# Kernel optimization log

Measured on AMD Instinct MI355X. Metric: run time of the kernel, lower is better.

## Reference

```python
import jax, jax.numpy as jnp
import numpy as np

H = 8        # num attention heads
DH = 160     # head dim (hidden_size // H)
HS = 1280    # hidden_size
CAD = 768    # cross_attention_dim
R = 4        # LoRA rank
LORA_SCALE = 1.0  # `scale` forward arg (default 1.0)


def setup_inputs() -> dict:
    key = jax.random.key(0)
    ks = jax.random.split(key, 16)
    rn = lambda k, s, std=0.02: (jax.random.normal(k, s) * std).astype(jnp.float32)
    return {
        "hidden_states": jax.random.normal(ks[0], (8, 4096, HS), jnp.float32),
        "encoder_hidden_states": jax.random.normal(ks[1], (8, 77, CAD), jnp.float32),
        # base attention projections (nn.Linear weight layout: [out, in])
        "Wq": rn(ks[2], (HS, HS)),
        "Wk": rn(ks[3], (HS, CAD)),
        "Wv": rn(ks[4], (HS, CAD)),
        "Wo": rn(ks[5], (HS, HS)),
        "bo": jnp.zeros((HS,), jnp.float32),
        # LoRA down/up pairs (down std ~ 1/rank; up nonzero so grads flow)
        "q_down": rn(ks[6], (R, HS), 0.25), "q_up": rn(ks[7], (HS, R)),
        "k_down": rn(ks[8], (R, CAD), 0.25), "k_up": rn(ks[9], (HS, R)),
        "v_down": rn(ks[10], (R, CAD), 0.25), "v_up": rn(ks[11], (HS, R)),
        "o_down": rn(ks[12], (R, HS), 0.25), "o_up": rn(ks[13], (HS, R)),
    }


def reference(hidden_states, encoder_hidden_states, Wq, Wk, Wv, Wo, bo,
              q_down, q_up, k_down, k_up, v_down, v_up, o_down, o_up):
    B, S, _ = hidden_states.shape
    T = encoder_hidden_states.shape[1]
    lora = lambda x, d, u: (x @ d.T) @ u.T  # LoRALinearLayer: up(down(x))

    q = hidden_states @ Wq.T + LORA_SCALE * lora(hidden_states, q_down, q_up)
    k = encoder_hidden_states @ Wk.T + LORA_SCALE * lora(encoder_hidden_states, k_down, k_up)
    v = encoder_hidden_states @ Wv.T + LORA_SCALE * lora(encoder_hidden_states, v_down, v_up)

    q = q.reshape(B, S, H, DH)
    k = k.reshape(B, T, H, DH)
    v = v.reshape(B, T, H, DH)

    # attn.get_attention_scores: scaled QK^T, softmax (no mask)
    inv_sqrt_d = jnp.asarray(1.0 / np.sqrt(DH), q.dtype)
    scores = jnp.einsum('bshd,bthd->bhst', q, k) * inv_sqrt_d
    probs = jax.nn.softmax(scores, axis=-1)
    o = jnp.einsum('bhst,bthd->bshd', probs, v).reshape(B, S, H * DH)

    # to_out[0] (Linear with bias) + LoRA on the same input; to_out[1] dropout = identity (eval)
    return o @ Wo.T + bo + LORA_SCALE * lora(o, o_down, o_up)
```

## Files before the change

kernel.cpp:

```cpp
#include <hip/hip_runtime.h>
#include <hip/hip_bf16.h>
#include <stdint.h>

typedef short bf16x8 __attribute__((ext_vector_type(8)));
typedef float f32x4 __attribute__((ext_vector_type(4)));

#define DEVI static __device__ __forceinline__

DEVI ushort f2bf(float f) {
  union { float f; uint32_t u; } v; v.f = f;
  uint32_t u = v.u;
  return (ushort)((u + 0x7fffu + ((u >> 16) & 1u)) >> 16);
}

DEVI void gload16(const void* g, void* l) {
  __builtin_amdgcn_global_load_lds((const __attribute__((address_space(1))) void*)g,
                                   (__attribute__((address_space(3))) void*)l,
                                   16, 0, 0);
}

#define SB() __builtin_amdgcn_sched_barrier(0)
#define BAR() __builtin_amdgcn_s_barrier()
#define MFMA(a, b, c) __builtin_amdgcn_mfma_f32_16x16x32_bf16((a), (b), (c), 0, 0, 0)

DEVI int pair_src_row(int c, int* k8) {
  int pair = c >> 3;
  int s = (c & 7) ^ (pair & 7);
  *k8 = s >> 1;
  return pair * 2 + (s & 1);
}
DEVI int pair_frag_off(int r, int k8) {
  int p = (k8 * 2 + (r & 1)) ^ ((r >> 1) & 7);
  return (r >> 1) * 64 + p * 8;
}

__global__ __launch_bounds__(256) void fold_t(
    const float* __restrict__ W, const float* __restrict__ up,
    const float* __restrict__ down, ushort* __restrict__ outT, float scale)
{
  __shared__ ushort tile[64][66];
  const int o0 = blockIdx.x * 64, i0 = blockIdx.y * 64;
  const int lo = threadIdx.x >> 6;
  const int li = threadIdx.x & 63;
#pragma unroll
  for (int r = 0; r < 16; ++r) {
    int o = o0 + r * 4 + lo;
    int i = i0 + li;
    float v = W[(long)o * 1280 + i];
#pragma unroll
    for (int q = 0; q < 4; ++q) v += up[o * 4 + q] * down[q * 1280 + i];
    tile[li][r * 4 + lo] = f2bf(v * scale);
  }
  __syncthreads();
#pragma unroll
  for (int r = 0; r < 16; ++r) {
    int i = i0 + r * 4 + lo;
    outT[(long)i * 1280 + o0 + li] = tile[r * 4 + lo][li];
  }
}

__global__ __launch_bounds__(256) void smalls(
    const float* __restrict__ ehs, ushort* __restrict__ ehs_bf,
    const float* __restrict__ Wk, const float* __restrict__ k_up, const float* __restrict__ k_down,
    const float* __restrict__ Wv, const float* __restrict__ v_up, const float* __restrict__ v_down,
    ushort* __restrict__ Wkv,
    const float* __restrict__ Wo, const float* __restrict__ o_up, const float* __restrict__ o_down,
    ushort* __restrict__ Wo_bf, ushort* __restrict__ Nt)
{
  const int b = blockIdx.x;
  const int tid = threadIdx.x;
  if (b < 231) {
    int idx = b * 256 + tid;
    if (idx < 59136) {
      const float4* p = (const float4*)(ehs + (long)idx * 8);
      float4 a = p[0], c = p[1];
      union { ushort us[8]; uint4 v; } r;
      r.us[0] = f2bf(a.x); r.us[1] = f2bf(a.y); r.us[2] = f2bf(a.z); r.us[3] = f2bf(a.w);
      r.us[4] = f2bf(c.x); r.us[5] = f2bf(c.y); r.us[6] = f2bf(c.z); r.us[7] = f2bf(c.w);
      *(uint4*)(ehs_bf + (long)idx * 8) = r.v;
    }
  } else if (b < 4071) {
    int idx = (b - 231) * 256 + tid;
    int o = idx / 768, i = idx - o * 768;
    float v = Wk[idx];
#pragma unroll
    for (int q = 0; q < 4; ++q) v += k_up[o * 4 + q] * k_down[q * 768 + i];
    Wkv[idx] = f2bf(v);
  } else if (b < 7911) {
    int idx = (b - 4071) * 256 + tid;
    int o = idx / 768, i = idx - o * 768;
    float v = Wv[idx];
#pragma unroll
    for (int q = 0; q < 4; ++q) v += v_up[o * 4 + q] * v_down[q * 768 + i];
    Wkv[983040 + idx] = f2bf(v);
  } else if (b < 14311) {
    int idx = (b - 7911) * 256 + tid;
    int o = idx / 1280, i = idx - o * 1280;
    float v = Wo[idx];
#pragma unroll
    for (int q = 0; q < 4; ++q) v += o_up[o * 4 + q] * o_down[q * 1280 + i];
    Wo_bf[idx] = f2bf(v);
  } else {
    int idx = (b - 14311) * 256 + tid;
    int bb = idx / (1280 * 24);
    int rem = idx % (1280 * 24);
    int j = rem / 24, q = rem % 24;
    int h = q / 3, t = 77 + q % 3;
    Nt[(long)bb * 1280 * 640 + (long)j * 640 + h * 80 + t] = 0;
  }
}


DEVI void gemm_bt_body(int bx, int by, int z,
    const ushort* __restrict__ A, long sA0, long sA1, int lda, int validM,
    const ushort* __restrict__ B, long sB0, long sB1, int ldb, int validN,
    float* __restrict__ C32, ushort* __restrict__ C16, long sC0, long sC1, int ldc,
    const float* __restrict__ bias, int K, ushort* As, ushort* Bs)
{
  const ushort* Ab = A + (long)(z >> 3) * sA0 + (long)(z & 7) * sA1;
  const ushort* Bb = B + (long)(z >> 3) * sB0 + (long)(z & 7) * sB1;
  const int m0 = bx * 128;
  const int n0 = by * 128;
  const int tid = threadIdx.x;
  const int lane = tid & 63;
  const int wid = tid >> 6;

  const int c0 = tid;
  const int arow0 = min(m0 + (c0 >> 2), validM - 1);
  const int arow1 = min(m0 + (c0 >> 2) + 64, validM - 1);
  const int brow0 = min(n0 + (c0 >> 2), validN - 1);
  const int brow1 = min(n0 + (c0 >> 2) + 64, validN - 1);
  const int seg = (c0 & 3) * 8;

  const int wr = (wid >> 1) * 64;
  const int wc = (wid & 1) * 64;
  const int frow = lane & 15;
  const int fk = (lane >> 4) * 8;

  f32x4 acc[4][4] = {};

  for (int kt = 0; kt < K; kt += 32) {
    gload16(Ab + (long)arow0 * lda + kt + seg, As + c0 * 8);
    gload16(Ab + (long)arow1 * lda + kt + seg, As + (c0 + 256) * 8);
    gload16(Bb + (long)brow0 * ldb + kt + seg, Bs + c0 * 8);
    gload16(Bb + (long)brow1 * ldb + kt + seg, Bs + (c0 + 256) * 8);
    __syncthreads();

    bf16x8 af[4], bfr[4];
#pragma unroll
    for (int m = 0; m < 4; ++m)
      af[m] = *(const bf16x8*)(As + (wr + m * 16 + frow) * 32 + fk);
#pragma unroll
    for (int n = 0; n < 4; ++n)
      bfr[n] = *(const bf16x8*)(Bs + (wc + n * 16 + frow) * 32 + fk);
#pragma unroll
    for (int m = 0; m < 4; ++m)
#pragma unroll
      for (int n = 0; n < 4; ++n)
        acc[m][n] = MFMA(af[m], bfr[n], acc[m][n]);
    __syncthreads();
  }

  const long cb = (long)(z >> 3) * sC0 + (long)(z & 7) * sC1;
  const int crow = m0 + wr + (lane >> 4) * 4;
  const int ccol = n0 + wc + (lane & 15);
#pragma unroll
  for (int m = 0; m < 4; ++m)
#pragma unroll
    for (int n = 0; n < 4; ++n)
#pragma unroll
      for (int j = 0; j < 4; ++j) {
        int r = crow + m * 16 + j;
        int c = ccol + n * 16;
        if (r < validM && c < validN) {
          float v = acc[m][n][j];
          if (bias) v += bias[c];
          if (C32) C32[cb + (long)r * ldc + c] = v;
          else     C16[cb + (long)r * ldc + c] = f2bf(v);
        }
      }
}

__global__ __launch_bounds__(256) void gemm_bt(
    const ushort* A, long sA0, long sA1, int lda, int validM,
    const ushort* B, long sB0, long sB1, int ldb, int validN,
    float* C32, ushort* C16, long sC0, long sC1, int ldc,
    const float* bias, int K)
{
  __shared__ ushort As[128 * 32];
  __shared__ ushort Bs[128 * 32];
  gemm_bt_body(blockIdx.x, blockIdx.y, blockIdx.z,
               A, sA0, sA1, lda, validM, B, sB0, sB1, ldb, validN,
               C32, C16, sC0, sC1, ldc, bias, K, As, Bs);
}

__global__ __launch_bounds__(256) void gemm_mtnt(
    const ushort* __restrict__ kv_bf, const ushort* __restrict__ WqT,
    const ushort* __restrict__ Wo_bf, ushort* __restrict__ Mt, ushort* __restrict__ Nt)
{
  __shared__ ushort As[128 * 32];
  __shared__ ushort Bs[128 * 32];
  const int x = blockIdx.x, z = blockIdx.z;
  if (x < 10) {
    gemm_bt_body(x, 0, z, Wo_bf, 0, 160, 1280, 1280,
                 kv_bf + 1280, 77L * 2560, 160, 2560, 77,
                 nullptr, Nt, 1280L * 640, 80, 640, nullptr, 160, As, Bs);
  } else {
    gemm_bt_body(0, x - 10, z, kv_bf, 77L * 2560, 160, 2560, 77,
                 WqT, 0, 160, 1280, 1280,
                 nullptr, Mt, 640L * 1280, 77L * 1280, 1280, nullptr, 160, As, Bs);
  }
}

__global__ __launch_bounds__(256, 3) void score_softmax(
    const float* __restrict__ hsf, const ushort* __restrict__ Mt,
    ushort* __restrict__ probs)
{
  __shared__ ushort lds[22528];

  const int z = blockIdx.z;
  const int s0 = blockIdx.x * 128;
  const int h0 = blockIdx.y * 2;
  const int tid = threadIdx.x;
  const int lane = tid & 63;
  const int wid = tid >> 6;
  const int wM = wid >> 1;
  const int wN = wid & 1;
  const int l15 = lane & 15;
  const int l4 = lane >> 4;

  const int ar = tid >> 1, ah = tid & 1;
  const float* Ag = hsf + ((long)z * 4096 + s0 + ar) * 1280 + 16 * ah;
  const int awoff0 = pair_frag_off(ar, 2 * ah);
  const int awoff1 = pair_frag_off(ar, 2 * ah + 1);

  const ushort* Bg = Mt + (long)z * (640L * 1280);
  long bsrc[3]; int bdst[3];
#pragma unroll
  for (int j = 0; j < 3; ++j) {
    int c = j * 256 + tid, k8;
    int rb = pair_src_row(c, &k8);
    int hh = h0 + (rb >= 96);
    int tt = min(rb - 96 * (rb >= 96), 76);
    bsrc[j] = (long)(hh * 77 + tt) * 1280 + k8 * 8;
    bdst[j] = 4096 + c * 8;
  }

  int aoff[4], boff[6];
#pragma unroll
  for (int m = 0; m < 4; ++m)
    aoff[m] = pair_frag_off(wM * 64 + m * 16 + l15, l4);
#pragma unroll
  for (int n = 0; n < 6; ++n)
    boff[n] = 4096 + pair_frag_off(wN * 96 + n * 16 + l15, l4);

  f32x4 acc[4][6] = {};
  float4 pa0, pa1, pa2, pa3;

#define SS_LOADA(kt) { const float* p_ = Ag + (kt); \
    pa0 = *(const float4*)(p_);     pa1 = *(const float4*)(p_ + 4); \
    pa2 = *(const float4*)(p_ + 8); pa3 = *(const float4*)(p_ + 12); }
#define SS_GLB(bb, kt) { _Pragma("unroll") for (int j = 0; j < 3; ++j) \
    gload16(Bg + bsrc[j] + (kt), &lds[(bb) + bdst[j]]); }
#define SS_CVTW(bb) { \
    union { ushort us[8]; bf16x8 v; } c0_, c1_; \
    c0_.us[0]=f2bf(pa0.x); c0_.us[1]=f2bf(pa0.y); c0_.us[2]=f2bf(pa0.z); c0_.us[3]=f2bf(pa0.w); \
    c0_.us[4]=f2bf(pa1.x); c0_.us[5]=f2bf(pa1.y); c0_.us[6]=f2bf(pa1.z); c0_.us[7]=f2bf(pa1.w); \
    c1_.us[0]=f2bf(pa2.x); c1_.us[1]=f2bf(pa2.y); c1_.us[2]=f2bf(pa2.z); c1_.us[3]=f2bf(pa2.w); \
    c1_.us[4]=f2bf(pa3.x); c1_.us[5]=f2bf(pa3.y); c1_.us[6]=f2bf(pa3.z); c1_.us[7]=f2bf(pa3.w); \
    *(bf16x8*)(&lds[(bb) + awoff0]) = c0_.v; \
    *(bf16x8*)(&lds[(bb) + awoff1]) = c1_.v; }

  SS_LOADA(0)
  SB();
  SS_GLB(0, 0)
  SB();
  SS_CVTW(0)
  asm volatile("s_waitcnt lgkmcnt(0)" ::: "memory");

  for (int t = 0; t < 40; ++t) {
    const int base = (t & 1) * 10240;
    const int nb = 10240 - base;
    if (t + 1 < 40) {
      const int kt1 = (t + 1) * 32;
      SS_LOADA(kt1)
      SB();
      SS_GLB(nb, kt1)
      asm volatile("s_waitcnt vmcnt(7)" ::: "memory");
    } else {
      asm volatile("s_waitcnt vmcnt(0)" ::: "memory");
    }
    SB(); BAR(); SB();
    bf16x8 av[4], bv[6];
#pragma unroll
    for (int m = 0; m < 4; ++m) av[m] = *(const bf16x8*)(&lds[base + aoff[m]]);
#pragma unroll
    for (int n = 0; n < 6; ++n) bv[n] = *(const bf16x8*)(&lds[base + boff[n]]);
    __builtin_amdgcn_s_setprio(1);
#pragma unroll
    for (int m = 0; m < 4; ++m)
#pragma unroll
      for (int n = 0; n < 6; ++n)
        acc[m][n] = MFMA(av[m], bv[n], acc[m][n]);
    __builtin_amdgcn_s_setprio(0);
    SB();
    if (t + 1 < 40) { SS_CVTW(nb) }
    asm volatile("s_waitcnt lgkmcnt(0)" ::: "memory");
    SB(); BAR();
  }
#undef SS_LOADA
#undef SS_GLB
#undef SS_CVTW

#pragma unroll
  for (int m = 0; m < 4; ++m)
#pragma unroll
    for (int j = 0; j < 4; ++j) {
      float mx = -1e30f;
#pragma unroll
      for (int n = 0; n < 6; ++n)
        if (n * 16 + l15 < 77) mx = fmaxf(mx, acc[m][n][j]);
#pragma unroll
      for (int o = 8; o; o >>= 1) mx = fmaxf(mx, __shfl_xor(mx, o));
      float sum = 0.f;
#pragma unroll
      for (int n = 0; n < 6; ++n) {
        float e = (n * 16 + l15 < 77) ? __expf(acc[m][n][j] - mx) : 0.f;
        acc[m][n][j] = e;
        sum += e;
      }
#pragma unroll
      for (int o = 8; o; o >>= 1) sum += __shfl_xor(sum, o);
      float inv = 1.f / sum;
#pragma unroll
      for (int n = 0; n < 6; ++n) acc[m][n][j] *= inv;
    }

  __syncthreads();
  ushort* pw = lds + wid * 5632;
#pragma unroll
  for (int m = 0; m < 4; ++m)
#pragma unroll
    for (int n = 0; n < 5; ++n)
#pragma unroll
      for (int j = 0; j < 4; ++j)
        pw[(m * 16 + l4 * 4 + j) * 88 + n * 16 + l15] = f2bf(acc[m][n][j]);

  const uint* pw32 = (const uint*)pw;
  uint* probs32 = (uint*)probs;
  const int head = h0 + wN;
  const long sbase = (long)z * 4096 + s0 + wM * 64;
#pragma unroll 4
  for (int k = 0; k < 40; ++k) {
    int f2 = k * 64 + lane;
    int r = f2 / 40;
    int tp = f2 - r * 40;
    probs32[(sbase + r) * 320 + head * 40 + tp] = pw32[r * 44 + tp];
  }
}

__global__ __launch_bounds__(256, 4) void gemm_out(
    const ushort* __restrict__ P, const ushort* __restrict__ Nt,
    float* __restrict__ C, const float* __restrict__ bias)
{
  __shared__ ushort lds[17408];

  const int z = blockIdx.z;
  const ushort* Ab = P + (long)z * (4096L * 640) + (long)blockIdx.x * 128 * 640;
  const ushort* Bb = Nt + (long)z * (1280L * 640) + (long)blockIdx.y * 128 * 640;
  const int tid = threadIdx.x;
  const int lane = tid & 63;
  const int wid = tid >> 6;
  const int wM = wid >> 1;
  const int wN = wid & 1;
  const int l15 = lane & 15;
  const int l4 = lane >> 4;

  long asrc[2]; int adst[2], bdst[2];
#pragma unroll
  for (int j = 0; j < 2; ++j) {
    int c = j * 256 + tid, k8;
    int r = pair_src_row(c, &k8);
    asrc[j] = (long)r * 640 + k8 * 8;
    adst[j] = c * 8;
    bdst[j] = 4096 + c * 8;
  }

  int aoff[4], boff[4];
#pragma unroll
  for (int m = 0; m < 4; ++m)
    aoff[m] = pair_frag_off(wM * 64 + m * 16 + l15, l4);
#pragma unroll
  for (int n = 0; n < 4; ++n)
    boff[n] = 4096 + pair_frag_off(wN * 64 + n * 16 + l15, l4);

  f32x4 acc[4][4] = {};

#define OG_STAGE(bb, kt) { \
    _Pragma("unroll") for (int j = 0; j < 2; ++j) gload16(Ab + asrc[j] + (kt), &lds[(bb) + adst[j]]); \
    _Pragma("unroll") for (int j = 0; j < 2; ++j) gload16(Bb + asrc[j] + (kt), &lds[(bb) + bdst[j]]); }

  OG_STAGE(0, 0)

  for (int t = 0; t < 20; ++t) {
    const int base = (t & 1) * 8192;
    if (t + 1 < 20) {
      OG_STAGE(8192 - base, (t + 1) * 32)
      asm volatile("s_waitcnt vmcnt(4)" ::: "memory");
    } else {
      asm volatile("s_waitcnt vmcnt(0)" ::: "memory");
    }
    SB(); BAR(); SB();
    bf16x8 av[4], bv[4];
#pragma unroll
    for (int m = 0; m < 4; ++m) av[m] = *(const bf16x8*)(&lds[base + aoff[m]]);
#pragma unroll
    for (int n = 0; n < 4; ++n) bv[n] = *(const bf16x8*)(&lds[base + boff[n]]);
    __builtin_amdgcn_s_setprio(1);
#pragma unroll
    for (int m = 0; m < 4; ++m)
#pragma unroll
      for (int n = 0; n < 4; ++n)
        acc[m][n] = MFMA(av[m], bv[n], acc[m][n]);
    __builtin_amdgcn_s_setprio(0);
    SB(); BAR();
  }
#undef OG_STAGE

  __syncthreads();
  float* pw = (float*)lds + wid * 1088;
  const int ccol = blockIdx.y * 128 + wN * 64;
  const float4 bv4 = *(const float4*)(bias + ccol + l15 * 4);
  const long crow0 = (long)z * 4096 + blockIdx.x * 128 + wM * 64;
#pragma unroll
  for (int m = 0; m < 4; ++m) {
#pragma unroll
    for (int n = 0; n < 4; ++n)
#pragma unroll
      for (int j = 0; j < 4; ++j)
        pw[(l4 * 4 + j) * 68 + n * 16 + l15] = acc[m][n][j];
    asm volatile("s_waitcnt lgkmcnt(0)" ::: "memory"); SB();
#pragma unroll
    for (int pass = 0; pass < 4; ++pass) {
      int r = pass * 4 + l4;
      float4 v = *(const float4*)(pw + r * 68 + l15 * 4);
      v.x += bv4.x; v.y += bv4.y; v.z += bv4.z; v.w += bv4.w;
      *(float4*)(C + (crow0 + m * 16 + r) * 1280 + ccol + l15 * 4) = v;
    }
    asm volatile("s_waitcnt lgkmcnt(0)" ::: "memory"); SB();
  }
}

extern "C" void kernel_launch(void* const* d_in, const int* in_sizes, int n_in,
                              void* d_out, int out_size, void* d_ws, size_t ws_size,
                              hipStream_t stream) {
  (void)in_sizes; (void)n_in; (void)out_size; (void)ws_size;
  const float* hs     = (const float*)d_in[0];
  const float* ehs    = (const float*)d_in[1];
  const float* Wq     = (const float*)d_in[2];
  const float* Wk     = (const float*)d_in[3];
  const float* Wv     = (const float*)d_in[4];
  const float* Wo     = (const float*)d_in[5];
  const float* bo     = (const float*)d_in[6];
  const float* q_down = (const float*)d_in[7];
  const float* q_up   = (const float*)d_in[8];
  const float* k_down = (const float*)d_in[9];
  const float* k_up   = (const float*)d_in[10];
  const float* v_down = (const float*)d_in[11];
  const float* v_up   = (const float*)d_in[12];
  const float* o_down = (const float*)d_in[13];
  const float* o_up   = (const float*)d_in[14];

  char* w = (char*)d_ws;
  size_t off = 0;
  auto alloc = [&](size_t b) { char* p = w + off; off = (off + b + 255) & ~(size_t)255; return p; };
  ushort* ehs_bf = (ushort*)alloc(616L * 768 * 2);
  ushort* WqT    = (ushort*)alloc(1280L * 1280 * 2);
  ushort* Wkv    = (ushort*)alloc(2560L * 768 * 2);
  ushort* Wo_bf  = (ushort*)alloc(1280L * 1280 * 2);
  ushort* kv_bf  = (ushort*)alloc(616L * 2560 * 2);
  ushort* Mt     = (ushort*)alloc(8L * 640 * 1280 * 2);
  ushort* Nt     = (ushort*)alloc(8L * 1280 * 640 * 2);
  ushort* probs  = (ushort*)alloc(8L * 4096 * 640 * 2);
  float*  outp   = (float*)d_out;
  const float invs = 0.07905694150420949f;

  fold_t<<<dim3(20, 20), 256, 0, stream>>>(Wq, q_up, q_down, WqT, invs);
  smalls<<<15271, 256, 0, stream>>>(ehs, ehs_bf,
      Wk, k_up, k_down, Wv, v_up, v_down, Wkv,
      Wo, o_up, o_down, Wo_bf, Nt);
  gemm_bt<<<dim3(5, 20, 1), 256, 0, stream>>>(ehs_bf, 0, 0, 768, 616,
      Wkv, 0, 0, 768, 2560, nullptr, kv_bf, 0, 0, 2560, nullptr, 768);
  gemm_mtnt<<<dim3(20, 1, 64), 256, 0, stream>>>(kv_bf, WqT, Wo_bf, Mt, Nt);
  score_softmax<<<dim3(32, 4, 8), 256, 0, stream>>>(hs, Mt, probs);
  gemm_out<<<dim3(32, 10, 8), 256, 0, stream>>>(probs, Nt, outp, bo);
}
```

Baseline: 285.2 us.

## Prefetch fp32 A tiles two steps ahead and use packed bf16 conversion

In score_softmax, the fp32 hidden-state A tile is now loaded two k-steps ahead into alternating register sets, while B still prefetches one step ahead. This gives global loads more time to land before conversion. Conversion uses the v_cvt_pk_bf16_f32 instruction in place of the manual rounding, and each thread now loads a pair-swizzled source row so its LDS store is a contiguous 16-byte write. The cost is extra live registers for the second prefetch buffer, which could hurt occupancy under launch_bounds(256,3).

```diff
diff --git a/kernel.cpp b/kernel.cpp
--- a/kernel.cpp
+++ b/kernel.cpp
@@ -11,6 +11,12 @@
   union { float f; uint32_t u; } v; v.f = f;
   uint32_t u = v.u;
   return (ushort)((u + 0x7fffu + ((u >> 16) & 1u)) >> 16);
+}
+
+DEVI uint cvtpk(float lo, float hi) {
+  uint r;
+  asm("v_cvt_pk_bf16_f32 %0, %1, %2" : "=v"(r) : "v"(lo), "v"(hi));
+  return r;
 }
 
 DEVI void gload16(const void* g, void* l) {
@@ -229,10 +235,12 @@
   const int l15 = lane & 15;
   const int l4 = lane >> 4;
 
-  const int ar = tid >> 1, ah = tid & 1;
-  const float* Ag = hsf + ((long)z * 4096 + s0 + ar) * 1280 + 16 * ah;
-  const int awoff0 = pair_frag_off(ar, 2 * ah);
-  const int awoff1 = pair_frag_off(ar, 2 * ah + 1);
+  const float* Ag = hsf + ((long)z * 4096 + s0) * 1280;
+  int ak0, ak1;
+  const int ar0 = pair_src_row(tid, &ak0);
+  const int ar1 = pair_src_row(tid + 256, &ak1);
+  const long asrc0 = (long)ar0 * 1280 + ak0 * 8;
+  const long asrc1 = (long)ar1 * 1280 + ak1 * 8;
 
   const ushort* Bg = Mt + (long)z * (640L * 1280);
   long bsrc[3]; int bdst[3];
@@ -255,59 +263,64 @@
     boff[n] = 4096 + pair_frag_off(wN * 96 + n * 16 + l15, l4);
 
   f32x4 acc[4][6] = {};
-  float4 pa0, pa1, pa2, pa3;
-
-#define SS_LOADA(kt) { const float* p_ = Ag + (kt); \
-    pa0 = *(const float4*)(p_);     pa1 = *(const float4*)(p_ + 4); \
-    pa2 = *(const float4*)(p_ + 8); pa3 = *(const float4*)(p_ + 12); }
+  float4 pa0 = {}, pa1 = {}, pa2 = {}, pa3 = {};
+  float4 pb0 = {}, pb1 = {}, pb2 = {}, pb3 = {};
+
+#define SS_LOADA(S0, S1, S2, S3, kt) { \
+    S0 = *(const float4*)(Ag + asrc0 + (kt)); S1 = *(const float4*)(Ag + asrc0 + (kt) + 4); \
+    S2 = *(const float4*)(Ag + asrc1 + (kt)); S3 = *(const float4*)(Ag + asrc1 + (kt) + 4); }
 #define SS_GLB(bb, kt) { _Pragma("unroll") for (int j = 0; j < 3; ++j) \
     gload16(Bg + bsrc[j] + (kt), &lds[(bb) + bdst[j]]); }
-#define SS_CVTW(bb) { \
-    union { ushort us[8]; bf16x8 v; } c0_, c1_; \
-    c0_.us[0]=f2bf(pa0.x); c0_.us[1]=f2bf(pa0.y); c0_.us[2]=f2bf(pa0.z); c0_.us[3]=f2bf(pa0.w); \
-    c0_.us[4]=f2bf(pa1.x); c0_.us[5]=f2bf(pa1.y); c0_.us[6]=f2bf(pa1.z); c0_.us[7]=f2bf(pa1.w); \
-    c1_.us[0]=f2bf(pa2.x); c1_.us[1]=f2bf(pa2.y); c1_.us[2]=f2bf(pa2.z); c1_.us[3]=f2bf(pa2.w); \
-    c1_.us[4]=f2bf(pa3.x); c1_.us[5]=f2bf(pa3.y); c1_.us[6]=f2bf(pa3.z); c1_.us[7]=f2bf(pa3.w); \
-    *(bf16x8*)(&lds[(bb) + awoff0]) = c0_.v; \
-    *(bf16x8*)(&lds[(bb) + awoff1]) = c1_.v; }
-
-  SS_LOADA(0)
+#define SS_CVTW(S0, S1, S2, S3, bb) { uint4 u_; \
+    u_.x = cvtpk(S0.x, S0.y); u_.y = cvtpk(S0.z, S0.w); \
+    u_.z = cvtpk(S1.x, S1.y); u_.w = cvtpk(S1.z, S1.w); \
+    *(uint4*)(&lds[(bb) + tid * 8]) = u_; \
+    u_.x = cvtpk(S2.x, S2.y); u_.y = cvtpk(S2.z, S2.w); \
+    u_.z = cvtpk(S3.x, S3.y); u_.w = cvtpk(S3.z, S3.w); \
+    *(uint4*)(&lds[(bb) + 2048 + tid * 8]) = u_; }
+
+#define SS_STEP(t, I0, I1, I2, I3, C0, C1, C2, C3) { \
+    const int base_ = ((t) & 1) * 10240; \
+    const int nb_ = 10240 - base_; \
+    if ((t) + 2 < 40) { \
+      SS_LOADA(I0, I1, I2, I3, ((t) + 2) * 32) \
+      SB(); \
+      SS_GLB(nb_, ((t) + 1) * 32) \
+      asm volatile("s_waitcnt vmcnt(7)" ::: "memory"); \
+    } else if ((t) + 1 < 40) { \
+      SS_GLB(nb_, ((t) + 1) * 32) \
+      asm volatile("s_waitcnt vmcnt(3)" ::: "memory"); \
+    } else { \
+      asm volatile("s_waitcnt vmcnt(0)" ::: "memory"); \
+    } \
+    SB(); BAR(); SB(); \
+    bf16x8 av_[4], bv_[6]; \
+    _Pragma("unroll") for (int m = 0; m < 4; ++m) av_[m] = *(const bf16x8*)(&lds[base_ + aoff[m]]); \
+    _Pragma("unroll") for (int n = 0; n < 6; ++n) bv_[n] = *(const bf16x8*)(&lds[base_ + boff[n]]); \
+    __builtin_amdgcn_s_setprio(1); \
+    _Pragma("unroll") for (int m = 0; m < 4; ++m) \
+      _Pragma("unroll") for (int n = 0; n < 6; ++n) \
+        acc[m][n] = MFMA(av_[m], bv_[n], acc[m][n]); \
+    __builtin_amdgcn_s_setprio(0); \
+    SB(); \
+    if ((t) + 1 < 40) { SS_CVTW(C0, C1, C2, C3, nb_) } \
+    asm volatile("s_waitcnt lgkmcnt(0)" ::: "memory"); \
+    SB(); BAR(); }
+
+  SS_LOADA(pa0, pa1, pa2, pa3, 0)
   SB();
   SS_GLB(0, 0)
   SB();
-  SS_CVTW(0)
+  SS_CVTW(pa0, pa1, pa2, pa3, 0)
+  SS_LOADA(pa0, pa1, pa2, pa3, 32)
+  SB();
   asm volatile("s_waitcnt lgkmcnt(0)" ::: "memory");
 
-  for (int t = 0; t < 40; ++t) {
-    const int base = (t & 1) * 10240;
-    const int nb = 10240 - base;
-    if (t + 1 < 40) {
-      const int kt1 = (t + 1) * 32;
-      SS_LOADA(kt1)
-      SB();
-      SS_GLB(nb, kt1)
-      asm volatile("s_waitcnt vmcnt(7)" ::: "memory");
-    } else {
-      asm volatile("s_waitcnt vmcnt(0)" ::: "memory");
-    }
-    SB(); BAR(); SB();
-    bf16x8 av[4], bv[6];
-#pragma unroll
-    for (int m = 0; m < 4; ++m) av[m] = *(const bf16x8*)(&lds[base + aoff[m]]);
-#pragma unroll
-    for (int n = 0; n < 6; ++n) bv[n] = *(const bf16x8*)(&lds[base + boff[n]]);
-    __builtin_amdgcn_s_setprio(1);
-#pragma unroll
-    for (int m = 0; m < 4; ++m)
-#pragma unroll
-      for (int n = 0; n < 6; ++n)
-        acc[m][n] = MFMA(av[m], bv[n], acc[m][n]);
-    __builtin_amdgcn_s_setprio(0);
-    SB();
-    if (t + 1 < 40) { SS_CVTW(nb) }
-    asm volatile("s_waitcnt lgkmcnt(0)" ::: "memory");
-    SB(); BAR();
-  }
+  for (int tt = 0; tt < 20; ++tt) {
+    SS_STEP(2 * tt,     pb0, pb1, pb2, pb3, pa0, pa1, pa2, pa3)
+    SS_STEP(2 * tt + 1, pa0, pa1, pa2, pa3, pb0, pb1, pb2, pb3)
+  }
+#undef SS_STEP
 #undef SS_LOADA
 #undef SS_GLB
 #undef SS_CVTW
```

After: 325.3 us. 14.1% more time.

## Pre-convert hidden states to bf16 and pad Mt to 80 rows per head

Applied to the files above, without the earlier changes.

A separate pass now converts hidden_states from fp32 to bf16, so score_softmax can stage both operands straight into LDS with direct global-to-LDS loads instead of loading fp32 into registers and converting inline. Mt is repacked with 80 rows per head, padding rows zeroed in the smalls kernel. The B tile therefore shrinks from 96 to 80 columns, which cuts MFMA work and LDS per block. The cost is an extra kernel that reads and writes the whole activation tensor.

```diff
diff --git a/kernel.cpp b/kernel.cpp
--- a/kernel.cpp
+++ b/kernel.cpp
@@ -32,6 +32,19 @@
 DEVI int pair_frag_off(int r, int k8) {
   int p = (k8 * 2 + (r & 1)) ^ ((r >> 1) & 7);
   return (r >> 1) * 64 + p * 8;
+}
+
+__global__ __launch_bounds__(256) void cvt_hs(const float* __restrict__ in,
+                                              ushort* __restrict__ out) {
+  const long step = 2048L * 256;
+  for (long idx = (long)blockIdx.x * 256 + threadIdx.x; idx < 5242880; idx += step) {
+    const float4* p = (const float4*)(in + idx * 8);
+    float4 a = p[0], b = p[1];
+    union { ushort us[8]; uint4 v; } r;
+    r.us[0] = f2bf(a.x); r.us[1] = f2bf(a.y); r.us[2] = f2bf(a.z); r.us[3] = f2bf(a.w);
+    r.us[4] = f2bf(b.x); r.us[5] = f2bf(b.y); r.us[6] = f2bf(b.z); r.us[7] = f2bf(b.w);
+    *(uint4*)(out + idx * 8) = r.v;
+  }
 }
 
 __global__ __launch_bounds__(256) void fold_t(
@@ -65,7 +78,7 @@
     const float* __restrict__ Wv, const float* __restrict__ v_up, const float* __restrict__ v_down,
     ushort* __restrict__ Wkv,
     const float* __restrict__ Wo, const float* __restrict__ o_up, const float* __restrict__ o_down,
-    ushort* __restrict__ Wo_bf, ushort* __restrict__ Nt)
+    ushort* __restrict__ Wo_bf, ushort* __restrict__ Nt, ushort* __restrict__ Mt)
 {
   const int b = blockIdx.x;
   const int tid = threadIdx.x;
@@ -100,13 +113,21 @@
 #pragma unroll
     for (int q = 0; q < 4; ++q) v += o_up[o * 4 + q] * o_down[q * 1280 + i];
     Wo_bf[idx] = f2bf(v);
-  } else {
+  } else if (b < 15271) {
     int idx = (b - 14311) * 256 + tid;
     int bb = idx / (1280 * 24);
     int rem = idx % (1280 * 24);
     int j = rem / 24, q = rem % 24;
     int h = q / 3, t = 77 + q % 3;
     Nt[(long)bb * 1280 * 640 + (long)j * 640 + h * 80 + t] = 0;
+  } else {
+    int idx = (b - 15271) * 256 + tid;
+    int bb = idx / 30720;
+    int rem = idx % 30720;
+    int h = rem / 3840;
+    int q = rem % 3840;
+    int p = q / 1280, i = q % 1280;
+    Mt[(long)bb * 819200 + (long)(h * 80 + 77 + p) * 1280 + i] = 0;
   }
 }
 
@@ -208,15 +229,15 @@
   } else {
     gemm_bt_body(0, x - 10, z, kv_bf, 77L * 2560, 160, 2560, 77,
                  WqT, 0, 160, 1280, 1280,
-                 nullptr, Mt, 640L * 1280, 77L * 1280, 1280, nullptr, 160, As, Bs);
+                 nullptr, Mt, 819200, 102400, 1280, nullptr, 160, As, Bs);
   }
 }
 
 __global__ __launch_bounds__(256, 3) void score_softmax(
-    const float* __restrict__ hsf, const ushort* __restrict__ Mt,
+    const ushort* __restrict__ hsb, const ushort* __restrict__ Mt,
     ushort* __restrict__ probs)
 {
-  __shared__ ushort lds[22528];
+  __shared__ ushort lds[23040];
 
   const int z = blockIdx.z;
   const int s0 = blockIdx.x * 128;
@@ -228,89 +249,67 @@
   const int wN = wid & 1;
   const int l15 = lane & 15;
   const int l4 = lane >> 4;
-
-  const int ar = tid >> 1, ah = tid & 1;
-  const float* Ag = hsf + ((long)z * 4096 + s0 + ar) * 1280 + 16 * ah;
-  const int awoff0 = pair_frag_off(ar, 2 * ah);
-  const int awoff1 = pair_frag_off(ar, 2 * ah + 1);
-
-  const ushort* Bg = Mt + (long)z * (640L * 1280);
-  long bsrc[3]; int bdst[3];
-#pragma unroll
-  for (int j = 0; j < 3; ++j) {
-    int c = j * 256 + tid, k8;
-    int rb = pair_src_row(c, &k8);
-    int hh = h0 + (rb >= 96);
-    int tt = min(rb - 96 * (rb >= 96), 76);
-    bsrc[j] = (long)(hh * 77 + tt) * 1280 + k8 * 8;
-    bdst[j] = 4096 + c * 8;
-  }
-
-  int aoff[4], boff[6];
+  const bool xb = tid < 128;
+
+  const ushort* Ag = hsb + ((long)z * 4096 + s0) * 1280;
+  int ak0, ak1;
+  const int ar0 = pair_src_row(tid, &ak0);
+  const int ar1 = pair_src_row(tid + 256, &ak1);
+  const long asrc0 = (long)ar0 * 1280 + ak0 * 8;
+  const long asrc1 = (long)ar1 * 1280 + ak1 * 8;
+  const ushort* Bg = Mt + (long)z * 819200 + (long)h0 * 80 * 1280;
+  int bk0, bk1, bk2;
+  const int br0 = pair_src_row(tid, &bk0);
+  const int br1 = pair_src_row(tid + 256, &bk1);
+  const int br2 = pair_src_row(tid + 512, &bk2);
+  const long bsrc0 = (long)br0 * 1280 + bk0 * 8;
+  const long bsrc1 = (long)br1 * 1280 + bk1 * 8;
+  const long bsrc2 = (long)br2 * 1280 + bk2 * 8;
+
+  int aoff[4], boff[5];
 #pragma unroll
   for (int m = 0; m < 4; ++m)
     aoff[m] = pair_frag_off(wM * 64 + m * 16 + l15, l4);
 #pragma unroll
-  for (int n = 0; n < 6; ++n)
-    boff[n] = 4096 + pair_frag_off(wN * 96 + n * 16 + l15, l4);
-
-  f32x4 acc[4][6] = {};
-  float4 pa0, pa1, pa2, pa3;
-
-#define SS_LOADA(kt) { const float* p_ = Ag + (kt); \
-    pa0 = *(const float4*)(p_);     pa1 = *(const float4*)(p_ + 4); \
-    pa2 = *(const float4*)(p_ + 8); pa3 = *(const float4*)(p_ + 12); }
-#define SS_GLB(bb, kt) { _Pragma("unroll") for (int j = 0; j < 3; ++j) \
-    gload16(Bg + bsrc[j] + (kt), &lds[(bb) + bdst[j]]); }
-#define SS_CVTW(bb) { \
-    union { ushort us[8]; bf16x8 v; } c0_, c1_; \
-    c0_.us[0]=f2bf(pa0.x); c0_.us[1]=f2bf(pa0.y); c0_.us[2]=f2bf(pa0.z); c0_.us[3]=f2bf(pa0.w); \
-    c0_.us[4]=f2bf(pa1.x); c0_.us[5]=f2bf(pa1.y); c0_.us[6]=f2bf(pa1.z); c0_.us[7]=f2bf(pa1.w); \
-    c1_.us[0]=f2bf(pa2.x); c1_.us[1]=f2bf(pa2.y); c1_.us[2]=f2bf(pa2.z); c1_.us[3]=f2bf(pa2.w); \
-    c1_.us[4]=f2bf(pa3.x); c1_.us[5]=f2bf(pa3.y); c1_.us[6]=f2bf(pa3.z); c1_.us[7]=f2bf(pa3.w); \
-    *(bf16x8*)(&lds[(bb) + awoff0]) = c0_.v; \
-    *(bf16x8*)(&lds[(bb) + awoff1]) = c1_.v; }
-
-  SS_LOADA(0)
-  SB();
-  SS_GLB(0, 0)
-  SB();
-  SS_CVTW(0)
-  asm volatile("s_waitcnt lgkmcnt(0)" ::: "memory");
+  for (int n = 0; n < 5; ++n)
+    boff[n] = 4096 + pair_frag_off(wN * 80 + n * 16 + l15, l4);
+
+  f32x4 acc[4][5] = {};
+
+#define SS_STAGE(bb, kt) { \
+    gload16(Ag + asrc0 + (kt), &lds[(bb) + tid * 8]); \
+    gload16(Ag + asrc1 + (kt), &lds[(bb) + 2048 + tid * 8]); \
+    gload16(Bg + bsrc0 + (kt), &lds[(bb) + 4096 + tid * 8]); \
+    gload16(Bg + bsrc1 + (kt), &lds[(bb) + 6144 + tid * 8]); \
+    if (xb) gload16(Bg + bsrc2 + (kt), &lds[(bb) + 8192 + tid * 8]); }
+
+  SS_STAGE(0, 0)
 
   for (int t = 0; t < 40; ++t) {
-    const int base = (t & 1) * 10240;
-    const int nb = 10240 - base;
+    const int base = (t & 1) * 9216;
     if (t + 1 < 40) {
-      const int kt1 = (t + 1) * 32;
-      SS_LOADA(kt1)
-      SB();
-      SS_GLB(nb, kt1)
-      asm volatile("s_waitcnt vmcnt(7)" ::: "memory");
+      SS_STAGE(9216 - base, (t + 1) * 32)
+      if (xb) { asm volatile("s_waitcnt vmcnt(5)" ::: "memory"); }
+      else    { asm volatile("s_waitcnt vmcnt(4)" ::: "memory"); }
     } else {
       asm volatile("s_waitcnt vmcnt(0)" ::: "memory");
     }
     SB(); BAR(); SB();
-    bf16x8 av[4], bv[6];
+    bf16x8 av[4], bv[5];
 #pragma unroll
     for (int m = 0; m < 4; ++m) av[m] = *(const bf16x8*)(&lds[base + aoff[m]]);
 #pragma unroll
-    for (int n = 0; n < 6; ++n) bv[n] = *(const bf16x8*)(&lds[base + boff[n]]);
+    for (int n = 0; n < 5; ++n) bv[n] = *(const bf16x8*)(&lds[base + boff[n]]);
     __builtin_amdgcn_s_setprio(1);
 #pragma unroll
     for (int m = 0; m < 4; ++m)
 #pragma unroll
-      for (int n = 0; n < 6; ++n)
+      for (int n = 0; n < 5; ++n)
         acc[m][n] = MFMA(av[m], bv[n], acc[m][n]);
     __builtin_amdgcn_s_setprio(0);
-    SB();
-    if (t + 1 < 40) { SS_CVTW(nb) }
-    asm volatile("s_waitcnt lgkmcnt(0)" ::: "memory");
     SB(); BAR();
   }
-#undef SS_LOADA
-#undef SS_GLB
-#undef SS_CVTW
+#undef SS_STAGE
 
 #pragma unroll
   for (int m = 0; m < 4; ++m)
@@ -318,13 +317,13 @@
     for (int j = 0; j < 4; ++j) {
       float mx = -1e30f;
 #pragma unroll
-      for (int n = 0; n < 6; ++n)
+      for (int n = 0; n < 5; ++n)
         if (n * 16 + l15 < 77) mx = fmaxf(mx, acc[m][n][j]);
 #pragma unroll
       for (int o = 8; o; o >>= 1) mx = fmaxf(mx, __shfl_xor(mx, o));
       float sum = 0.f;
 #pragma unroll
-      for (int n = 0; n < 6; ++n) {
+      for (int n = 0; n < 5; ++n) {
         float e = (n * 16 + l15 < 77) ? __expf(acc[m][n][j] - mx) : 0.f;
         acc[m][n][j] = e;
         sum += e;
@@ -333,18 +332,18 @@
       for (int o = 8; o; o >>= 1) sum += __shfl_xor(sum, o);
       float inv = 1.f / sum;
 #pragma unroll
-      for (int n = 0; n < 6; ++n) acc[m][n][j] *= inv;
+      for (int n = 0; n < 5; ++n) acc[m][n][j] *= inv;
     }
 
   __syncthreads();
-  ushort* pw = lds + wid * 5632;
+  ushort* pw = lds + wid * 5760;
 #pragma unroll
   for (int m = 0; m < 4; ++m)
 #pragma unroll
     for (int n = 0; n < 5; ++n)
 #pragma unroll
       for (int j = 0; j < 4; ++j)
-        pw[(m * 16 + l4 * 4 + j) * 88 + n * 16 + l15] = f2bf(acc[m][n][j]);
+        pw[(m * 16 + l4 * 4 + j) * 90 + n * 16 + l15] = f2bf(acc[m][n][j]);
 
   const uint* pw32 = (const uint*)pw;
   uint* probs32 = (uint*)probs;
@@ -355,7 +354,7 @@
     int f2 = k * 64 + lane;
     int r = f2 / 40;
     int tp = f2 - r * 40;
-    probs32[(sbase + r) * 320 + head * 40 + tp] = pw32[r * 44 + tp];
+    probs32[(sbase + r) * 320 + head * 40 + tp] = pw32[r * 45 + tp];
   }
 }
 
@@ -474,6 +473,7 @@
   char* w = (char*)d_ws;
   size_t off = 0;
   auto alloc = [&](size_t b) { char* p = w + off; off = (off + b + 255) & ~(size_t)255; return p; };
+  ushort* hs_bf  = (ushort*)alloc(32768L * 1280 * 2);
   ushort* ehs_bf = (ushort*)alloc(616L * 768 * 2);
   ushort* WqT    = (ushort*)alloc(1280L * 1280 * 2);
   ushort* Wkv    = (ushort*)alloc(2560L * 768 * 2);
@@ -485,13 +485,14 @@
   float*  outp   = (float*)d_out;
   const float invs = 0.07905694150420949f;
 
+  cvt_hs<<<2048, 256, 0, stream>>>(hs, hs_bf);
   fold_t<<<dim3(20, 20), 256, 0, stream>>>(Wq, q_up, q_down, WqT, invs);
-  smalls<<<15271, 256, 0, stream>>>(ehs, ehs_bf,
+  smalls<<<16231, 256, 0, stream>>>(ehs, ehs_bf,
       Wk, k_up, k_down, Wv, v_up, v_down, Wkv,
-      Wo, o_up, o_down, Wo_bf, Nt);
+      Wo, o_up, o_down, Wo_bf, Nt, Mt);
   gemm_bt<<<dim3(5, 20, 1), 256, 0, stream>>>(ehs_bf, 0, 0, 768, 616,
       Wkv, 0, 0, 768, 2560, nullptr, kv_bf, 0, 0, 2560, nullptr, 768);
   gemm_mtnt<<<dim3(20, 1, 64), 256, 0, stream>>>(kv_bf, WqT, Wo_bf, Mt, Nt);
-  score_softmax<<<dim3(32, 4, 8), 256, 0, stream>>>(hs, Mt, probs);
+  score_softmax<<<dim3(32, 4, 8), 256, 0, stream>>>(hs_bf, Mt, probs);
   gemm_out<<<dim3(32, 10, 8), 256, 0, stream>>>(probs, Nt, outp, bo);
 }
```

After: 278.4 us, median of 2. 1.02x faster.
